# Kernel tuning notes

Hardware: AMD Instinct MI355X
Metric: run time of the kernel (lower is better)

## Reference

```python
import jax, jax.numpy as jnp
import numpy as np

SIZE = 4096
NB = 16            # nr_blocks_per_row
NDROP = 8          # nr_blocks_to_drop_per_row
BATCH = 8192
BLOCK = SIZE // NB # 256


def _block_mask():
    # latin_square(n): S[i,j] = ((i+j) mod n) + 1, values 1..n, each once per row/col
    i = np.arange(NB)
    S = ((i[:, None] + i[None, :]) % NB) + 1
    m = S > NDROP  # keep NB-NDROP blocks per row
    mask = np.repeat(np.repeat(m, BLOCK, axis=0), BLOCK, axis=1)
    return jnp.asarray(mask)  # [SIZE, SIZE] bool


def setup_inputs() -> dict:
    key = jax.random.key(0)
    kx, kw, kb = jax.random.split(key, 3)
    x = jax.random.normal(kx, (BATCH, SIZE), dtype=jnp.float32)
    # kaiming_normal_ default: fan_in mode, relu gain -> std = sqrt(2/fan_in)
    weight = jax.random.normal(kw, (SIZE, SIZE), dtype=jnp.float32) * jnp.sqrt(2.0 / SIZE)
    # uniform(-1,1) scaled by sqrt(1/size)
    bias = jax.random.uniform(kb, (SIZE,), minval=-1.0, maxval=1.0, dtype=jnp.float32) * jnp.sqrt(1.0 / SIZE)
    mask = _block_mask()
    return {"x": x, "weight": weight, "bias": bias, "mask": mask}


def reference(x, weight, bias, mask):
    # x @ (mask * weight).T + bias
    w = jnp.where(mask, weight, jnp.zeros((), dtype=weight.dtype))
    return x @ w.T + bias
```

## Files before the change

### kernel.cpp

```cpp
#include <hip/hip_runtime.h>
#include <hip/hip_bf16.h>
#include <stdint.h>


typedef __bf16 bf16x8 __attribute__((ext_vector_type(8)));
typedef float  f32x4  __attribute__((ext_vector_type(4)));

#define AS1 __attribute__((address_space(1)))
#define AS3 __attribute__((address_space(3)))

__device__ __forceinline__ void async_cp16(const void* g, void* l) {
  __builtin_amdgcn_global_load_lds((const AS1 void*)g, (AS3 void*)l, 16, 0, 0);
}

__device__ __forceinline__ uint32_t pack_bf16(float a, float b) {
  uint32_t ua = __float_as_uint(a);
  ua += 0x7fffu + ((ua >> 16) & 1u);
  uint32_t ub = __float_as_uint(b);
  ub += 0x7fffu + ((ub >> 16) & 1u);
  return (ua >> 16) | (ub & 0xffff0000u);
}

__global__ __launch_bounds__(256) void cvt_x(const float* __restrict__ x,
                                             uint2* __restrict__ xb) {
  const int t = threadIdx.x;
  const int b = blockIdx.x;
  const float4* p = (const float4*)(x + (size_t)b * 4096);
  uint2* o = xb + (size_t)b * 1024;
  float4 a0 = p[t];
  float4 a1 = p[t + 256];
  float4 a2 = p[t + 512];
  float4 a3 = p[t + 768];
  o[t]       = make_uint2(pack_bf16(a0.x, a0.y), pack_bf16(a0.z, a0.w));
  o[t + 256] = make_uint2(pack_bf16(a1.x, a1.y), pack_bf16(a1.z, a1.w));
  o[t + 512] = make_uint2(pack_bf16(a2.x, a2.y), pack_bf16(a2.z, a2.w));
  o[t + 768] = make_uint2(pack_bf16(a3.x, a3.y), pack_bf16(a3.z, a3.w));
}

__global__ __launch_bounds__(256) void cvt_w(const float* __restrict__ w,
                                             uint2* __restrict__ wb) {
  const int t = threadIdx.x;
  const int n = blockIdx.x;
  const int kstart = ((8 - (n >> 8)) & 15) << 8;
  const float* src = w + (size_t)n * 4096;
  uint2* dst = wb + (size_t)n * 512;
  float4 a0 = *(const float4*)(src + ((kstart + 4 * t) & 4095));
  float4 a1 = *(const float4*)(src + ((kstart + 1024 + 4 * t) & 4095));
  dst[t]       = make_uint2(pack_bf16(a0.x, a0.y), pack_bf16(a0.z, a0.w));
  dst[t + 256] = make_uint2(pack_bf16(a1.x, a1.y), pack_bf16(a1.z, a1.w));
}

__global__ __launch_bounds__(256, 2) void gemm_bs(
    const uint16_t* __restrict__ X,
    const uint16_t* __restrict__ W,
    const float* __restrict__ bias,
    float* __restrict__ out) {
  constexpr int K = 4096;
  __shared__ uint16_t sA[128 * 32];
  __shared__ uint16_t sB[128 * 32];

  const int tid = threadIdx.x;
  const int lin = blockIdx.x;
  const int q = lin >> 3;
  const int bn = ((lin & 7) << 2) + (q & 3);
  const int bm = q >> 2;
  const int m0 = bm << 7;
  const int n0 = bn << 7;
  const int bi = bn >> 1;

  const int tr = tid >> 2;
  const int tc = (((tid & 3) ^ ((tr >> 1) & 3)) << 3);
  const uint16_t* gA0 = X + (size_t)(m0 + tr) * K + tc;
  const uint16_t* gA1 = X + (size_t)(m0 + 64 + tr) * K + tc;
  const uint16_t* gB0 = W + (size_t)(n0 + tr) * 2048 + tc;
  const uint16_t* gB1 = W + (size_t)(n0 + 64 + tr) * 2048 + tc;
  uint16_t* lA0 = sA + tid * 8;
  uint16_t* lA1 = sA + 2048 + tid * 8;
  uint16_t* lB0 = sB + tid * 8;
  uint16_t* lB1 = sB + 2048 + tid * 8;

  const int lane = tid & 63;
  const int wv = tid >> 6;
  const int wm = (wv >> 1) << 6;
  const int wn = (wv & 1) << 6;
  const int fr = lane & 15;
  const int slotx = (((lane >> 4) ^ ((fr >> 1) & 3)) << 3);

  f32x4 acc[4][4];
#pragma unroll
  for (int i = 0; i < 4; ++i)
#pragma unroll
    for (int j = 0; j < 4; ++j)
      acc[i][j] = (f32x4){0.f, 0.f, 0.f, 0.f};

  for (int t = 0; t < 8; ++t) {
    const int kbA = ((24 + t - bi) & 15) << 8;
    const int kbB = t << 8;
#pragma unroll
    for (int u = 0; u < 8; ++u) {
      const int kA = kbA + (u << 5);
      const int kB = kbB + (u << 5);
      __syncthreads();
      async_cp16(gA0 + kA, lA0);
      async_cp16(gA1 + kA, lA1);
      async_cp16(gB0 + kB, lB0);
      async_cp16(gB1 + kB, lB1);
      __syncthreads();

      bf16x8 av[4], bv[4];
#pragma unroll
      for (int i = 0; i < 4; ++i)
        av[i] = *(const bf16x8*)(sA + ((wm + (i << 4) + fr) << 5) + slotx);
#pragma unroll
      for (int j = 0; j < 4; ++j)
        bv[j] = *(const bf16x8*)(sB + ((wn + (j << 4) + fr) << 5) + slotx);
#pragma unroll
      for (int i = 0; i < 4; ++i)
#pragma unroll
        for (int j = 0; j < 4; ++j)
          acc[i][j] = __builtin_amdgcn_mfma_f32_16x16x32_bf16(av[i], bv[j],
                                                              acc[i][j], 0, 0, 0);
    }
  }

  const int rq = (lane >> 4) << 2;
#pragma unroll
  for (int j = 0; j < 4; ++j) {
    const int c = n0 + wn + (j << 4) + fr;
    const float bz = bias[c];
#pragma unroll
    for (int i = 0; i < 4; ++i) {
      const int r0 = m0 + wm + (i << 4) + rq;
#pragma unroll
      for (int r = 0; r < 4; ++r)
        out[(size_t)(r0 + r) * 4096 + c] = acc[i][j][r] + bz;
    }
  }
}

extern "C" void kernel_launch(void* const* d_in, const int* in_sizes, int n_in,
                              void* d_out, int out_size, void* d_ws, size_t ws_size,
                              hipStream_t stream) {
  const float* x = (const float*)d_in[0];
  const float* w = (const float*)d_in[1];
  const float* bias = (const float*)d_in[2];
  float* out = (float*)d_out;

  uint16_t* xb = (uint16_t*)d_ws;
  uint16_t* wb = xb + (size_t)8192 * 4096;

  hipLaunchKernelGGL(cvt_x, dim3(8192), dim3(256), 0, stream, x, (uint2*)xb);
  hipLaunchKernelGGL(cvt_w, dim3(4096), dim3(256), 0, stream, w, (uint2*)wb);

  hipLaunchKernelGGL(gemm_bs, dim3(2048), dim3(256), 0, stream,
                     xb, wb, bias, out);
}
```

Before: 437.6 us.

## Rewrite block-sparse GEMM as 256x256 tile, 8-wave, double-buffered pipelined kernel

Replaces the 128x128 single-buffered GEMM with a 256x256-tile, 512-thread kernel using 128KB of LDS and double buffering. Global-to-LDS async copies of the next K-slice overlap MFMA compute in four quadrant phases, with explicit vmcnt waits, barriers and setprio. The larger tile and 64-wide K step increase data reuse and cut barriers per FLOP. The cost is heavy LDS use, which limits occupancy, and only 512 workgroups, which may underfill the GPU.

```diff
diff --git a/kernel.cpp b/kernel.cpp
--- a/kernel.cpp
+++ b/kernel.cpp
@@ -50,87 +50,131 @@
   dst[t + 256] = make_uint2(pack_bf16(a1.x, a1.y), pack_bf16(a1.z, a1.w));
 }
 
-__global__ __launch_bounds__(256, 2) void gemm_bs(
+__global__ __launch_bounds__(512, 2) void gemm_bs8(
     const uint16_t* __restrict__ X,
     const uint16_t* __restrict__ W,
     const float* __restrict__ bias,
     float* __restrict__ out) {
-  constexpr int K = 4096;
-  __shared__ uint16_t sA[128 * 32];
-  __shared__ uint16_t sB[128 * 32];
+  __shared__ char L[131072];
 
   const int tid = threadIdx.x;
   const int lin = blockIdx.x;
-  const int q = lin >> 3;
-  const int bn = ((lin & 7) << 2) + (q & 3);
-  const int bm = q >> 2;
-  const int m0 = bm << 7;
-  const int n0 = bn << 7;
-  const int bi = bn >> 1;
-
-  const int tr = tid >> 2;
-  const int tc = (((tid & 3) ^ ((tr >> 1) & 3)) << 3);
-  const uint16_t* gA0 = X + (size_t)(m0 + tr) * K + tc;
-  const uint16_t* gA1 = X + (size_t)(m0 + 64 + tr) * K + tc;
-  const uint16_t* gB0 = W + (size_t)(n0 + tr) * 2048 + tc;
-  const uint16_t* gB1 = W + (size_t)(n0 + 64 + tr) * 2048 + tc;
-  uint16_t* lA0 = sA + tid * 8;
-  uint16_t* lA1 = sA + 2048 + tid * 8;
-  uint16_t* lB0 = sB + tid * 8;
-  uint16_t* lB1 = sB + 2048 + tid * 8;
+  const int xcd = lin & 7;
+  const int idx = lin >> 3;
+  const int bm = idx >> 1;
+  const int bn = (xcd << 1) + (idx & 1);
+  const int m0 = bm << 8;
+  const int n0 = bn << 8;
+  const int kstart = ((8 - bn) & 15) << 8;
+
+  const int chswz = (((tid & 7) ^ ((tid >> 4) & 7)) << 3);
+  const uint16_t* Xb = X + (size_t)(m0 + (tid >> 3)) * 4096 + chswz;
+  const uint16_t* Wb = W + (size_t)(n0 + ((tid >> 8) << 6) + ((tid >> 3) & 31)) * 2048 + chswz;
+  char* dA = L + tid * 16;
+  char* dB = L + 32768 + tid * 16;
+
+  auto stageA = [&](int buf, int q, int s) {
+    const size_t gk = (size_t)((kstart + (s << 6)) & 4095);
+    const uint16_t* s0 = Xb + (size_t)(q << 6) * 4096 + gk;
+    char* d = dA + (buf << 16) + (q << 13);
+    async_cp16(s0, d);
+    async_cp16(s0 + (size_t)128 * 4096, d + 16384);
+  };
+  auto stageB = [&](int buf, int b, int s) {
+    const uint16_t* s0 = Wb + (size_t)(b << 5) * 2048 + (s << 6);
+    char* d = dB + (buf << 16) + (b << 14);
+    async_cp16(s0, d);
+    async_cp16(s0 + (size_t)128 * 2048, d + 8192);
+  };
 
   const int lane = tid & 63;
   const int wv = tid >> 6;
-  const int wm = (wv >> 1) << 6;
-  const int wn = (wv & 1) << 6;
+  const int wmh = wv >> 2;
+  const int wnq = wv & 3;
   const int fr = lane & 15;
-  const int slotx = (((lane >> 4) ^ ((fr >> 1) & 3)) << 3);
-
-  f32x4 acc[4][4];
-#pragma unroll
-  for (int i = 0; i < 4; ++i)
+  const int g = lane >> 4;
+  const int fsw = (fr >> 1) & 7;
+  const int sl0 = ((g ^ fsw) << 4);
+  const int sl1 = (((g + 4) ^ fsw) << 4);
+  const int aoff = wmh * 16384 + fr * 128;
+  const int boff = 32768 + wnq * 4096 + fr * 128;
+
+  f32x4 acc[8][4];
+#pragma unroll
+  for (int i = 0; i < 8; ++i)
 #pragma unroll
     for (int j = 0; j < 4; ++j)
       acc[i][j] = (f32x4){0.f, 0.f, 0.f, 0.f};
 
-  for (int t = 0; t < 8; ++t) {
-    const int kbA = ((24 + t - bi) & 15) << 8;
-    const int kbB = t << 8;
-#pragma unroll
-    for (int u = 0; u < 8; ++u) {
-      const int kA = kbA + (u << 5);
-      const int kB = kbB + (u << 5);
-      __syncthreads();
-      async_cp16(gA0 + kA, lA0);
-      async_cp16(gA1 + kA, lA1);
-      async_cp16(gB0 + kB, lB0);
-      async_cp16(gB1 + kB, lB1);
-      __syncthreads();
-
-      bf16x8 av[4], bv[4];
-#pragma unroll
-      for (int i = 0; i < 4; ++i)
-        av[i] = *(const bf16x8*)(sA + ((wm + (i << 4) + fr) << 5) + slotx);
-#pragma unroll
-      for (int j = 0; j < 4; ++j)
-        bv[j] = *(const bf16x8*)(sB + ((wn + (j << 4) + fr) << 5) + slotx);
-#pragma unroll
-      for (int i = 0; i < 4; ++i)
-#pragma unroll
-        for (int j = 0; j < 4; ++j)
-          acc[i][j] = __builtin_amdgcn_mfma_f32_16x16x32_bf16(av[i], bv[j],
-                                                              acc[i][j], 0, 0, 0);
-    }
+#define VMW(N) asm volatile("s_waitcnt vmcnt(" #N ")" ::: "memory")
+
+#define PHASE(BUF, QM, QN, WAITSTMT, STAGE)                                   \
+  {                                                                           \
+    const int ab = ((BUF) << 16) + aoff + (QM) * 8192;                        \
+    const int bb = ((BUF) << 16) + boff + (QN) * 16384;                       \
+    bf16x8 av[4][2], bv[2][2];                                                \
+    _Pragma("unroll")                                                         \
+    for (int i = 0; i < 4; ++i) {                                             \
+      av[i][0] = *(const bf16x8*)(L + ab + i * 2048 + sl0);                   \
+      av[i][1] = *(const bf16x8*)(L + ab + i * 2048 + sl1);                   \
+    }                                                                         \
+    _Pragma("unroll")                                                         \
+    for (int j = 0; j < 2; ++j) {                                             \
+      bv[j][0] = *(const bf16x8*)(L + bb + j * 2048 + sl0);                   \
+      bv[j][1] = *(const bf16x8*)(L + bb + j * 2048 + sl1);                   \
+    }                                                                         \
+    STAGE;                                                                    \
+    __builtin_amdgcn_s_barrier();                                             \
+    asm volatile("s_waitcnt lgkmcnt(0)" ::: "memory");                        \
+    __builtin_amdgcn_sched_barrier(0);                                        \
+    __builtin_amdgcn_s_setprio(1);                                            \
+    _Pragma("unroll")                                                         \
+    for (int i = 0; i < 4; ++i)                                               \
+      _Pragma("unroll")                                                       \
+      for (int j = 0; j < 2; ++j) {                                           \
+        acc[(QM) * 4 + i][(QN) * 2 + j] =                                     \
+            __builtin_amdgcn_mfma_f32_16x16x32_bf16(                          \
+                av[i][0], bv[j][0], acc[(QM) * 4 + i][(QN) * 2 + j], 0, 0, 0);\
+        acc[(QM) * 4 + i][(QN) * 2 + j] =                                     \
+            __builtin_amdgcn_mfma_f32_16x16x32_bf16(                          \
+                av[i][1], bv[j][1], acc[(QM) * 4 + i][(QN) * 2 + j], 0, 0, 0);\
+      }                                                                       \
+    __builtin_amdgcn_s_setprio(0);                                            \
+    WAITSTMT;                                                                 \
+    __builtin_amdgcn_s_barrier();                                             \
   }
 
-  const int rq = (lane >> 4) << 2;
+  stageA(0, 0, 0);
+  stageB(0, 0, 0);
+  stageB(0, 1, 0);
+  stageA(0, 1, 0);
+  asm volatile("s_waitcnt vmcnt(0)" ::: "memory");
+  __builtin_amdgcn_s_barrier();
+
+  for (int t = 0; t < 31; ++t) {
+    const int buf = t & 1;
+    const int nb = buf ^ 1;
+    const int s1 = t + 1;
+    PHASE(buf, 0, 0, VMW(4), stageA(nb, 0, s1));
+    PHASE(buf, 0, 1, VMW(4), stageB(nb, 0, s1));
+    PHASE(buf, 1, 0, (void)0, stageB(nb, 1, s1));
+    PHASE(buf, 1, 1, VMW(4), stageA(nb, 1, s1));
+  }
+  PHASE(1, 0, 0, VMW(2), (void)0);
+  PHASE(1, 0, 1, VMW(0), (void)0);
+  PHASE(1, 1, 0, (void)0, (void)0);
+  PHASE(1, 1, 1, (void)0, (void)0);
+#undef PHASE
+#undef VMW
+
+  const int rq = g << 2;
 #pragma unroll
   for (int j = 0; j < 4; ++j) {
-    const int c = n0 + wn + (j << 4) + fr;
+    const int c = n0 + wnq * 64 + ((j >> 1) << 5) + ((j & 1) << 4) + fr;
     const float bz = bias[c];
 #pragma unroll
-    for (int i = 0; i < 4; ++i) {
-      const int r0 = m0 + wm + (i << 4) + rq;
+    for (int i = 0; i < 8; ++i) {
+      const int r0 = m0 + wmh * 128 + ((i >> 2) << 6) + ((i & 3) << 4) + rq;
 #pragma unroll
       for (int r = 0; r < 4; ++r)
         out[(size_t)(r0 + r) * 4096 + c] = acc[i][j][r] + bz;
@@ -152,6 +196,6 @@
   hipLaunchKernelGGL(cvt_x, dim3(8192), dim3(256), 0, stream, x, (uint2*)xb);
   hipLaunchKernelGGL(cvt_w, dim3(4096), dim3(256), 0, stream, w, (uint2*)wb);
 
-  hipLaunchKernelGGL(gemm_bs, dim3(2048), dim3(256), 0, stream,
+  hipLaunchKernelGGL(gemm_bs8, dim3(512), dim3(512), 0, stream,
                      xb, wb, bias, out);
 }
```

New measurement: 430.1 us. Within noise of the previous version (-1.7%).
